# Optimization experiments

Measured on AMD Instinct MI355X. Metric: run time of the kernel, lower is better.

## Reference

```python
import jax, jax.numpy as jnp
import numpy as np

NUM_GROUPS = 32
EPS = 1e-6


def group_norm(x, gamma, beta):
    b, c, h, w = x.shape
    xg = x.reshape(b, NUM_GROUPS, c // NUM_GROUPS, h, w)
    mean = jnp.mean(xg, axis=(2, 3, 4), keepdims=True)
    var = jnp.var(xg, axis=(2, 3, 4), keepdims=True)
    xg = (xg - mean) * jax.lax.rsqrt(var + EPS)
    x = xg.reshape(b, c, h, w)
    return x * gamma[None, :, None, None] + beta[None, :, None, None]


def conv1x1(x, w, b):
    # x: [B,C,H,W], w: [Cout,Cin], b: [Cout]
    return jnp.einsum('bchw,oc->bohw', x, w) + b[None, :, None, None]


def setup_inputs() -> dict:
    key = jax.random.key(0)
    ks = jax.random.split(key, 11)
    B, C, H, W = 2, 512, 64, 64
    s = 1.0 / np.sqrt(C)
    return {
        'x': jax.random.normal(ks[0], (B, C, H, W), jnp.float32),
        'norm_gamma': jnp.ones((C,), jnp.float32),
        'norm_beta': jnp.zeros((C,), jnp.float32),
        'wq': jax.random.normal(ks[1], (C, C), jnp.float32) * s,
        'bq': jnp.zeros((C,), jnp.float32),
        'wk': jax.random.normal(ks[2], (C, C), jnp.float32) * s,
        'bk': jnp.zeros((C,), jnp.float32),
        'wv': jax.random.normal(ks[3], (C, C), jnp.float32) * s,
        'bv': jnp.zeros((C,), jnp.float32),
        'wo': jax.random.normal(ks[4], (C, C), jnp.float32) * s,
        'bo': jnp.zeros((C,), jnp.float32),
    }


def reference(x, norm_gamma, norm_beta, wq, bq, wk, bk, wv, bv, wo, bo):
    b, c, h, w = x.shape
    hn = group_norm(x, norm_gamma, norm_beta)
    q = conv1x1(hn, wq, bq).reshape(b, c, h * w)  # [B,C,HW]
    k = conv1x1(hn, wk, bk).reshape(b, c, h * w)
    v = conv1x1(hn, wv, bv).reshape(b, c, h * w)
    scale = jnp.asarray(c, x.dtype) ** -0.5
    # scores[b,i,j] = sum_c q[b,c,i] * k[b,c,j]
    scores = jnp.einsum('bci,bcj->bij', q, k) * scale
    attn = jax.nn.softmax(scores, axis=2)
    # out[b,c,i] = sum_j v[b,c,j] * attn[b,i,j]
    out = jnp.einsum('bcj,bij->bci', v, attn).reshape(b, c, h, w)
    out = conv1x1(out, wo, bo)
    return x + out
```

## Files before the change

### kernel.cpp

```cpp
#include <hip/hip_runtime.h>
#include <hip/hip_bf16.h>

using u16 = unsigned short;
typedef __attribute__((ext_vector_type(4))) float f32x4;
typedef __attribute__((ext_vector_type(8))) __bf16 bf16x8;
typedef __attribute__((ext_vector_type(8))) short s16x8;
typedef __attribute__((ext_vector_type(4))) short s16x4;

#define DEVI __device__ __forceinline__

constexpr int BATCH = 2, C = 512, HW = 4096, NG = 32, CPG = 16;

DEVI float b2f(u16 u) { union { unsigned u; float f; } a; a.u = ((unsigned)u) << 16; return a.f; }
DEVI u16 f2b(float f) {
  union { float f; unsigned u; } a; a.f = f;
  unsigned r = a.u + 0x7fffu + ((a.u >> 16) & 1u);
  return (u16)(r >> 16);
}

__global__ __launch_bounds__(256) void cvt_w(const float* __restrict__ a, const float* __restrict__ b,
                                             const float* __restrict__ c, const float* __restrict__ d,
                                             u16* __restrict__ out) {
  int i = blockIdx.x * 256 + threadIdx.x;
  int w = i >> 16;
  int off = (i & 65535) * 4;
  const float* s = (w == 0) ? a : (w == 1) ? b : (w == 2) ? c : d;
  f32x4 v = *(const f32x4*)(s + off);
  s16x4 o;
  o[0] = (short)f2b(v[0]); o[1] = (short)f2b(v[1]); o[2] = (short)f2b(v[2]); o[3] = (short)f2b(v[3]);
  *(s16x4*)(out + (size_t)w * 262144 + off) = o;
}

__global__ __launch_bounds__(1024) void gn_stats(const float* __restrict__ x, float* __restrict__ stats) {
  int bg = blockIdx.x;
  const f32x4* xg = (const f32x4*)(x + (size_t)bg * (CPG * HW));
  float s = 0.f, ss = 0.f;
  for (int i = threadIdx.x; i < CPG * HW / 4; i += 1024) {
    f32x4 v = xg[i];
    s += v[0] + v[1] + v[2] + v[3];
    ss += v[0] * v[0] + v[1] * v[1] + v[2] * v[2] + v[3] * v[3];
  }
  #pragma unroll
  for (int o = 32; o; o >>= 1) { s += __shfl_xor(s, o); ss += __shfl_xor(ss, o); }
  __shared__ float red[32];
  int wv = threadIdx.x >> 6, ln = threadIdx.x & 63;
  if (ln == 0) { red[wv] = s; red[16 + wv] = ss; }
  __syncthreads();
  if (threadIdx.x == 0) {
    float S = 0.f, SS = 0.f;
    for (int i = 0; i < 16; ++i) { S += red[i]; SS += red[16 + i]; }
    float inv = 1.f / (float)(CPG * HW);
    float mean = S * inv;
    float var = SS * inv - mean * mean;
    stats[bg * 2] = mean;
    stats[bg * 2 + 1] = rsqrtf(var + 1e-6f);
  }
}

__global__ __launch_bounds__(256) void gn_normT(const float* __restrict__ x, const float* __restrict__ stats,
                                                const float* __restrict__ gamma, const float* __restrict__ beta,
                                                u16* __restrict__ hnT) {
  __shared__ u16 tile[64][66];
  int b = blockIdx.z, c0 = blockIdx.y * 64, h0 = blockIdx.x * 64;
  int t = threadIdx.x;
  const float* xb = x + ((size_t)b * C + c0) * HW + h0;
  int r = t / 16, cc = (t % 16) * 4;
  #pragma unroll
  for (int it = 0; it < 4; ++it) {
    int rr = it * 16 + r;
    int ch = c0 + rr;
    int g = b * NG + (ch >> 4);
    float mean = stats[g * 2], rstd = stats[g * 2 + 1];
    float ga = gamma[ch] * rstd;
    float be = beta[ch] - mean * ga;
    f32x4 v = *(const f32x4*)(xb + (size_t)rr * HW + cc);
    #pragma unroll
    for (int j = 0; j < 4; ++j) tile[rr][cc + j] = f2b(v[j] * ga + be);
  }
  __syncthreads();
  u16* op = hnT + (size_t)b * HW * C + (size_t)h0 * C + c0;
  int hr2 = t / 8, cg = (t % 8) * 8;
  #pragma unroll
  for (int it = 0; it < 2; ++it) {
    int hr = it * 32 + hr2;
    s16x8 o8;
    #pragma unroll
    for (int j = 0; j < 8; ++j) o8[j] = (short)tile[cg + j][hr];
    *(s16x8*)(op + (size_t)hr * C + cg) = o8;
  }
}

#define EPI_BIAS_M 1
#define EPI_BIAS_N 2
#define EPI_RESID  4
#define EPI_F32OUT 8

template <int EPI>
__global__ __launch_bounds__(256) void gemm_bt(const u16* __restrict__ A, const u16* __restrict__ Bt,
                                               void* __restrict__ Co, int M, int N, int K,
                                               long long sA, long long sB, long long sC,
                                               const float* __restrict__ bias,
                                               const float* __restrict__ resid, long long sR) {
  (void)M;
  __shared__ u16 ldsA[128 * 64];
  __shared__ u16 ldsB[128 * 64];
  const int tid = threadIdx.x;
  const int bz = blockIdx.z;
  const int bm = blockIdx.y, bn = blockIdx.x;
  A += (size_t)bz * sA;
  Bt += (size_t)bz * sB;
  const int wave = tid >> 6, lane = tid & 63;
  const int wr = wave >> 1, wc = wave & 1;
  f32x4 acc[4][4] = {};

  const int srow = tid >> 3;
  const int sch = (tid & 7) ^ (srow & 7);
  const u16* gA = A + (size_t)(bm * 128 + srow) * K + sch * 8;
  const u16* gB = Bt + (size_t)(bn * 128 + srow) * K + sch * 8;
  u16* lA = ldsA + wave * 512;
  u16* lB = ldsB + wave * 512;

  for (int k0 = 0; k0 < K; k0 += 64) {
    #pragma unroll
    for (int cc = 0; cc < 4; ++cc) {
      __builtin_amdgcn_global_load_lds(
          (const __attribute__((address_space(1))) void*)(gA + (size_t)cc * 32 * K + k0),
          (__attribute__((address_space(3))) void*)(lA + cc * 2048), 16, 0, 0);
      __builtin_amdgcn_global_load_lds(
          (const __attribute__((address_space(1))) void*)(gB + (size_t)cc * 32 * K + k0),
          (__attribute__((address_space(3))) void*)(lB + cc * 2048), 16, 0, 0);
    }
    __syncthreads();
    #pragma unroll
    for (int kk = 0; kk < 2; ++kk) {
      bf16x8 af[4], bfv[4];
      #pragma unroll
      for (int m = 0; m < 4; ++m) {
        int r = wr * 64 + m * 16 + (lane & 15);
        int chunk = (kk * 4 + (lane >> 4)) ^ (r & 7);
        af[m] = *(const bf16x8*)(ldsA + r * 64 + chunk * 8);
      }
      #pragma unroll
      for (int n = 0; n < 4; ++n) {
        int r = wc * 64 + n * 16 + (lane & 15);
        int chunk = (kk * 4 + (lane >> 4)) ^ (r & 7);
        bfv[n] = *(const bf16x8*)(ldsB + r * 64 + chunk * 8);
      }
      #pragma unroll
      for (int m = 0; m < 4; ++m)
        #pragma unroll
        for (int n = 0; n < 4; ++n)
          acc[m][n] = __builtin_amdgcn_mfma_f32_16x16x32_bf16(af[m], bfv[n], acc[m][n], 0, 0, 0);
    }
    __syncthreads();
  }

  const int col0 = bn * 128 + wc * 64;
  const int row0 = bm * 128 + wr * 64 + ((lane >> 4) << 2);
  #pragma unroll
  for (int m = 0; m < 4; ++m) {
    #pragma unroll
    for (int j = 0; j < 4; ++j) {
      int gm = row0 + m * 16 + j;
      float bm_v = (EPI & EPI_BIAS_M) ? bias[gm] : 0.f;
      #pragma unroll
      for (int n = 0; n < 4; ++n) {
        int gn = col0 + n * 16 + (lane & 15);
        float v = acc[m][n][j] + bm_v;
        if (EPI & EPI_BIAS_N) v += bias[gn];
        if (EPI & EPI_RESID) v += resid[(size_t)bz * sR + (size_t)gm * N + gn];
        if (EPI & EPI_F32OUT)
          ((float*)Co)[(size_t)bz * sC + (size_t)gm * N + gn] = v;
        else
          ((u16*)Co)[(size_t)bz * sC + (size_t)gm * N + gn] = f2b(v);
      }
    }
  }
}

template <bool SCALED>
__global__ __launch_bounds__(512, 2) void gemm256(
    const u16* __restrict__ Ag, const u16* __restrict__ Bg,
    u16* __restrict__ Co, u16* __restrict__ Co2, int zSwitch,
    int Nld, int ldK, int nsplitLog, int kLen,
    long long sA, long long sB, long long sC, float scale) {
  __shared__ u16 lds[65536];
  const int tid = threadIdx.x;
  const int lane = tid & 63, w = tid >> 6;
  const int wm = w >> 2, wn = w & 3;
  const int l15 = lane & 15, l4 = lane >> 4;
  const int bn = blockIdx.x, bm = blockIdx.y;
  const int z = blockIdx.z;
  const int bz = z >> nsplitLog, kz = z & ((1 << nsplitLog) - 1);
  const int kStart = kz * kLen;
  const int NT = kLen >> 6;

  const int rStage = w * 8 + (lane >> 3);
  const int gch = (lane & 7) ^ (lane >> 3);
  const u16* gA = Ag + (size_t)bz * sA + (size_t)(bm * 256) * ldK + kStart + gch * 8;
  const u16* gB = Bg + (size_t)bz * sB + (size_t)(bn * 256) * ldK + kStart + gch * 8;

  f32x4 acc[8][4] = {};
  bf16x8 aF[4][2], bF[2][2][2];

  const int hB = wn >> 1, qB = wn & 1;
  const u16* pA0 = lds + (0 * 4 + wm) * 8192;
  const u16* pA1 = lds + (1 * 4 + wm) * 8192;
  const u16* pB0 = lds + (0 * 4 + 2 + hB) * 8192;
  const u16* pB1 = lds + (1 * 4 + 2 + hB) * 8192;

  #define STAGE(TT, DB, AB, HF) { \
    const u16* gbase = (AB) ? gB : gA; \
    u16* l0 = lds + ((DB) * 4 + (AB) * 2 + (HF)) * 8192 + w * 512; \
    _Pragma("unroll") for (int s = 0; s < 2; ++s) { \
      const u16* gp = gbase + (size_t)((HF) * 128 + s * 64 + rStage) * ldK + (TT) * 64; \
      __builtin_amdgcn_global_load_lds((const __attribute__((address_space(1))) void*)gp, \
          (__attribute__((address_space(3))) void*)(l0 + s * 4096), 16, 0, 0); } }

  #define LOAD_A(P, MH) { _Pragma("unroll") for (int j = 0; j < 4; ++j) \
    _Pragma("unroll") for (int kk = 0; kk < 2; ++kk) { \
      const int r_ = (MH) * 64 + j * 16 + l15; const int c_ = (kk * 4 + l4) ^ (r_ & 7); \
      aF[j][kk] = *(const bf16x8*)((P) + r_ * 64 + c_ * 8); } }

  #define LOAD_B(P, NH) { _Pragma("unroll") for (int j = 0; j < 2; ++j) \
    _Pragma("unroll") for (int kk = 0; kk < 2; ++kk) { \
      const int r_ = qB * 64 + (NH) * 32 + j * 16 + l15; const int c_ = (kk * 4 + l4) ^ (r_ & 7); \
      bF[NH][j][kk] = *(const bf16x8*)((P) + r_ * 64 + c_ * 8); } }

  #define MM(MH, NH) { __builtin_amdgcn_s_setprio(1); \
    _Pragma("unroll") for (int j = 0; j < 4; ++j) \
      _Pragma("unroll") for (int j2 = 0; j2 < 2; ++j2) \
        _Pragma("unroll") for (int kk = 0; kk < 2; ++kk) \
          acc[(MH) * 4 + j][(NH) * 2 + j2] = __builtin_amdgcn_mfma_f32_16x16x32_bf16( \
              aF[j][kk], bF[NH][j2][kk], acc[(MH) * 4 + j][(NH) * 2 + j2], 0, 0, 0); \
    __builtin_amdgcn_s_setprio(0); }

  #define BAR __builtin_amdgcn_s_barrier()
  #define WLG { asm volatile("s_waitcnt lgkmcnt(0)" ::: "memory"); __builtin_amdgcn_sched_barrier(0); }
  #define WV4 asm volatile("s_waitcnt vmcnt(4)" ::: "memory")
  #define WV0 asm volatile("s_waitcnt vmcnt(0)" ::: "memory")

  STAGE(0, 0, 1, 0); STAGE(0, 0, 1, 1);
  STAGE(0, 0, 0, 0); STAGE(0, 0, 0, 1);
  STAGE(1, 1, 1, 0); STAGE(1, 1, 1, 1);
  WV4; BAR;

  const int NI = NT / 2 - 1;
  for (int i = 0; i < NI; ++i) {
    const int t1 = 2 * i + 1, u0 = 2 * i + 2, u1 = 2 * i + 3;
    LOAD_A(pA0, 0); LOAD_B(pB0, 0); STAGE(t1, 1, 0, 0); BAR; WLG; MM(0, 0); BAR;
    LOAD_B(pB0, 1); STAGE(t1, 1, 0, 1); BAR; WLG; MM(0, 1); BAR;
    LOAD_A(pA0, 1); STAGE(u0, 0, 1, 0); BAR; WLG; MM(1, 1); BAR;
    STAGE(u0, 0, 1, 1); BAR; WLG; MM(1, 0); WV4; BAR;
    LOAD_A(pA1, 0); LOAD_B(pB1, 0); STAGE(u0, 0, 0, 0); BAR; WLG; MM(0, 0); BAR;
    LOAD_B(pB1, 1); STAGE(u0, 0, 0, 1); BAR; WLG; MM(0, 1); BAR;
    LOAD_A(pA1, 1); STAGE(u1, 1, 1, 0); BAR; WLG; MM(1, 1); BAR;
    STAGE(u1, 1, 1, 1); BAR; WLG; MM(1, 0); WV4; BAR;
  }
  {
    const int t1 = NT - 1;
    LOAD_A(pA0, 0); LOAD_B(pB0, 0); STAGE(t1, 1, 0, 0); BAR; WLG; MM(0, 0); BAR;
    LOAD_B(pB0, 1); STAGE(t1, 1, 0, 1); BAR; WLG; MM(0, 1); BAR;
    LOAD_A(pA0, 1); BAR; WLG; MM(1, 1); BAR;
    BAR; WLG; MM(1, 0); WV0; BAR;
    LOAD_A(pA1, 0); LOAD_B(pB1, 0); BAR; WLG; MM(0, 0); BAR;
    LOAD_B(pB1, 1); BAR; WLG; MM(0, 1); BAR;
    LOAD_A(pA1, 1); BAR; WLG; MM(1, 1); BAR;
    MM(1, 0);
  }
  #undef STAGE
  #undef LOAD_A
  #undef LOAD_B
  #undef MM
  #undef BAR
  #undef WLG
  #undef WV4
  #undef WV0

  u16* outp = (z < zSwitch) ? (Co + (size_t)z * sC) : (Co2 + (size_t)(z - zSwitch) * sC);
  const int gm0 = bm * 256 + wm * 128 + l4 * 4;
  const int gn0 = bn * 256 + wn * 64 + l15;
  #pragma unroll
  for (int m = 0; m < 8; ++m) {
    #pragma unroll
    for (int j = 0; j < 4; ++j) {
      const size_t rowoff = (size_t)(gm0 + m * 16 + j) * Nld;
      #pragma unroll
      for (int n = 0; n < 4; ++n) {
        float v = acc[m][n][j];
        if (SCALED) v *= scale;
        outp[rowoff + gn0 + n * 16] = f2b(v);
      }
    }
  }
}

__global__ __launch_bounds__(256) void softmax_rows(u16* __restrict__ S) {
  int row = blockIdx.x * 4 + (threadIdx.x >> 6);
  int lane = threadIdx.x & 63;
  s16x8* p = (s16x8*)(S + (size_t)row * 4096);
  float v[64];
  float m = -1e30f;
  #pragma unroll
  for (int j = 0; j < 8; ++j) {
    s16x8 raw = p[j * 64 + lane];
    #pragma unroll
    for (int e = 0; e < 8; ++e) {
      float f = b2f((u16)raw[e]);
      v[j * 8 + e] = f;
      m = fmaxf(m, f);
    }
  }
  #pragma unroll
  for (int o = 32; o; o >>= 1) m = fmaxf(m, __shfl_xor(m, o));
  float s = 0.f;
  #pragma unroll
  for (int i = 0; i < 64; ++i) { v[i] = __expf(v[i] - m); s += v[i]; }
  #pragma unroll
  for (int o = 32; o; o >>= 1) s += __shfl_xor(s, o);
  float r = 1.f / s;
  #pragma unroll
  for (int j = 0; j < 8; ++j) {
    s16x8 o8;
    #pragma unroll
    for (int e = 0; e < 8; ++e) o8[e] = (short)f2b(v[j * 8 + e] * r);
    p[j * 64 + lane] = o8;
  }
}

__global__ __launch_bounds__(256) void reduce_pv(const u16* __restrict__ P, const u16* __restrict__ P2,
                                                 u16* __restrict__ ao) {
  const size_t e = ((size_t)blockIdx.x * 256 + threadIdx.x) * 8;
  const int b = (int)(e >> 21);
  const size_t o = e & 2097151;
  float s[8] = {0.f, 0.f, 0.f, 0.f, 0.f, 0.f, 0.f, 0.f};
  #pragma unroll
  for (int kz = 0; kz < 4; ++kz) {
    const int zz = b * 4 + kz;
    const u16* src = (zz < 6) ? (P + (size_t)zz * 2097152) : (P2 + (size_t)(zz - 6) * 2097152);
    s16x8 v = *(const s16x8*)(src + o);
    #pragma unroll
    for (int j = 0; j < 8; ++j) s[j] += b2f((u16)v[j]);
  }
  s16x8 o8;
  #pragma unroll
  for (int j = 0; j < 8; ++j) o8[j] = (short)f2b(s[j]);
  *(s16x8*)(ao + e) = o8;
}

extern "C" void kernel_launch(void* const* d_in, const int* in_sizes, int n_in,
                              void* d_out, int out_size, void* d_ws, size_t ws_size,
                              hipStream_t stream) {
  (void)in_sizes; (void)n_in; (void)out_size; (void)ws_size;
  const float* x     = (const float*)d_in[0];
  const float* gamma = (const float*)d_in[1];
  const float* beta  = (const float*)d_in[2];
  const float* wq    = (const float*)d_in[3];
  const float* bq    = (const float*)d_in[4];
  const float* wk    = (const float*)d_in[5];
  const float* bk    = (const float*)d_in[6];
  const float* wv    = (const float*)d_in[7];
  const float* bv    = (const float*)d_in[8];
  const float* wo    = (const float*)d_in[9];
  const float* bo    = (const float*)d_in[10];

  char* ws = (char*)d_ws;
  const size_t MiB = 1024 * 1024;
  float* stats = (float*)ws;
  u16* wbf = (u16*)(ws + 1024);
  u16* vv  = (u16*)(ws + 4 * MiB);
  u16* hnT = (u16*)(ws + 12 * MiB);
  u16* qT  = (u16*)(ws + 20 * MiB);
  u16* kT  = (u16*)(ws + 28 * MiB);
  u16* Ppart = (u16*)(ws + 12 * MiB);
  u16* Sm  = (u16*)(ws + 36 * MiB);
  u16* aoT = (u16*)(ws + 36 * MiB);

  const long long sTok = (long long)HW * C;
  const long long sS   = (long long)HW * HW;
  const float scale = 0.044194173824159216f;

  cvt_w<<<dim3(1024), dim3(256), 0, stream>>>(wq, wk, wv, wo, wbf);
  gn_stats<<<dim3(64), dim3(1024), 0, stream>>>(x, stats);
  gn_normT<<<dim3(HW / 64, C / 64, BATCH), dim3(256), 0, stream>>>(x, stats, gamma, beta, hnT);

  gemm_bt<EPI_BIAS_N><<<dim3(4, 32, BATCH), dim3(256), 0, stream>>>(
      hnT, wbf + 0 * 262144, qT, HW, C, C, sTok, 0, sTok, bq, nullptr, 0);
  gemm_bt<EPI_BIAS_N><<<dim3(4, 32, BATCH), dim3(256), 0, stream>>>(
      hnT, wbf + 1 * 262144, kT, HW, C, C, sTok, 0, sTok, bk, nullptr, 0);
  gemm_bt<EPI_BIAS_M><<<dim3(32, 4, BATCH), dim3(256), 0, stream>>>(
      wbf + 2 * 262144, hnT, vv, C, HW, C, 0, sTok, sTok, bv, nullptr, 0);

  gemm256<true><<<dim3(16, 16, BATCH), dim3(512), 0, stream>>>(
      qT, kT, Sm, Sm, 1000, HW, C, 0, C, sTok, sTok, sS, scale);

  softmax_rows<<<dim3(2048), dim3(256), 0, stream>>>(Sm);

  gemm256<false><<<dim3(2, 16, BATCH * 4), dim3(512), 0, stream>>>(
      Sm, vv, Ppart, (u16*)d_out, 6, C, HW, 2, HW / 4, sS, sTok, (long long)2097152, 1.f);

  reduce_pv<<<dim3(2048), dim3(256), 0, stream>>>(Ppart, (const u16*)d_out, aoT);

  gemm_bt<EPI_BIAS_M | EPI_RESID | EPI_F32OUT><<<dim3(32, 4, BATCH), dim3(256), 0, stream>>>(
      wbf + 3 * 262144, aoT, d_out, C, HW, C, 0, sTok, (long long)C * HW, bo, x, (long long)C * HW);
}
```

Before: 190.7 us.

## Fuse Q/K projections, remap workgroups across XCDs, stage gemm256 epilogue through LDS

Q and K projections now run as one GEMM against the concatenated wq|wk weights, writing an interleaved [HW,1024] buffer. This removes a launch and a second read of hnT. All GEMMs remap flat block IDs so that consecutive tiles land on the same XCD, which should improve L2 reuse. The 256x256 GEMM epilogue now writes to swizzled LDS and then stores coalesced 16-byte vectors instead of scattered 2-byte stores. The costs are wider strides for the QK^T reads and an extra LDS round trip with a barrier.

Result: faster. 178.9 us (-6.2%).

```diff
diff --git a/kernel.cpp b/kernel.cpp
--- a/kernel.cpp
+++ b/kernel.cpp
@@ -16,6 +16,18 @@
   union { float f; unsigned u; } a; a.f = f;
   unsigned r = a.u + 0x7fffu + ((a.u >> 16) & 1u);
   return (u16)(r >> 16);
+}
+
+DEVI void xcd_remap(int& bx, int& by, int& bz) {
+  const int nx = gridDim.x, ny = gridDim.y;
+  const int nwg = nx * ny * gridDim.z;
+  const int flat = blockIdx.x + nx * (blockIdx.y + ny * blockIdx.z);
+  const int cpx = nwg >> 3;
+  const int w = (flat & 7) * cpx + (flat >> 3);
+  bx = w % nx;
+  const int t = w / nx;
+  by = t % ny;
+  bz = t / ny;
 }
 
 __global__ __launch_bounds__(256) void cvt_w(const float* __restrict__ a, const float* __restrict__ b,
@@ -94,19 +106,21 @@
 #define EPI_BIAS_N 2
 #define EPI_RESID  4
 #define EPI_F32OUT 8
+#define EPI_QK     32
 
 template <int EPI>
 __global__ __launch_bounds__(256) void gemm_bt(const u16* __restrict__ A, const u16* __restrict__ Bt,
                                                void* __restrict__ Co, int M, int N, int K,
                                                long long sA, long long sB, long long sC,
                                                const float* __restrict__ bias,
+                                               const float* __restrict__ biasB,
                                                const float* __restrict__ resid, long long sR) {
   (void)M;
   __shared__ u16 ldsA[128 * 64];
   __shared__ u16 ldsB[128 * 64];
   const int tid = threadIdx.x;
-  const int bz = blockIdx.z;
-  const int bm = blockIdx.y, bn = blockIdx.x;
+  int bn, bm, bz;
+  xcd_remap(bn, bm, bz);
   A += (size_t)bz * sA;
   Bt += (size_t)bz * sB;
   const int wave = tid >> 6, lane = tid & 63;
@@ -167,7 +181,10 @@
       for (int n = 0; n < 4; ++n) {
         int gn = col0 + n * 16 + (lane & 15);
         float v = acc[m][n][j] + bm_v;
-        if (EPI & EPI_BIAS_N) v += bias[gn];
+        if (EPI & EPI_BIAS_N) {
+          if (EPI & EPI_QK) v += (gn < 512) ? bias[gn] : biasB[gn - 512];
+          else v += bias[gn];
+        }
         if (EPI & EPI_RESID) v += resid[(size_t)bz * sR + (size_t)gm * N + gn];
         if (EPI & EPI_F32OUT)
           ((float*)Co)[(size_t)bz * sC + (size_t)gm * N + gn] = v;
@@ -189,8 +206,8 @@
   const int lane = tid & 63, w = tid >> 6;
   const int wm = w >> 2, wn = w & 3;
   const int l15 = lane & 15, l4 = lane >> 4;
-  const int bn = blockIdx.x, bm = blockIdx.y;
-  const int z = blockIdx.z;
+  int bn, bm, z;
+  xcd_remap(bn, bm, z);
   const int bz = z >> nsplitLog, kz = z & ((1 << nsplitLog) - 1);
   const int kStart = kz * kLen;
   const int NT = kLen >> 6;
@@ -277,20 +294,32 @@
   #undef WV4
   #undef WV0
 
-  u16* outp = (z < zSwitch) ? (Co + (size_t)z * sC) : (Co2 + (size_t)(z - zSwitch) * sC);
-  const int gm0 = bm * 256 + wm * 128 + l4 * 4;
-  const int gn0 = bn * 256 + wn * 64 + l15;
-  #pragma unroll
-  for (int m = 0; m < 8; ++m) {
-    #pragma unroll
-    for (int j = 0; j < 4; ++j) {
-      const size_t rowoff = (size_t)(gm0 + m * 16 + j) * Nld;
+  {
+    const int rloc = wm * 128 + l4 * 4;
+    const int cloc = wn * 64 + l15;
+    #pragma unroll
+    for (int m = 0; m < 8; ++m) {
       #pragma unroll
-      for (int n = 0; n < 4; ++n) {
-        float v = acc[m][n][j];
-        if (SCALED) v *= scale;
-        outp[rowoff + gn0 + n * 16] = f2b(v);
+      for (int j = 0; j < 4; ++j) {
+        const int r_ = rloc + m * 16 + j;
+        const int xr = ((r_ >> 2) & 3) << 5;
+        #pragma unroll
+        for (int n = 0; n < 4; ++n) {
+          float v = acc[m][n][j];
+          if (SCALED) v *= scale;
+          *(u16*)((char*)lds + ((r_ * 512 + (cloc + n * 16) * 2) ^ xr)) = f2b(v);
+        }
       }
+    }
+    __syncthreads();
+    u16* outp = (z < zSwitch) ? (Co + (size_t)z * sC) : (Co2 + (size_t)(z - zSwitch) * sC);
+    #pragma unroll
+    for (int it = 0; it < 16; ++it) {
+      const int idx = it * 512 + tid;
+      const int r_ = idx >> 5, ch = idx & 31;
+      const int xr = ((r_ >> 2) & 3) << 5;
+      s16x8 d8 = *(const s16x8*)((const char*)lds + ((r_ * 512 + ch * 16) ^ xr));
+      *(s16x8*)(outp + (size_t)(bm * 256 + r_) * Nld + bn * 256 + ch * 8) = d8;
     }
   }
 }
@@ -369,30 +398,28 @@
   float* stats = (float*)ws;
   u16* wbf = (u16*)(ws + 1024);
   u16* vv  = (u16*)(ws + 4 * MiB);
-  u16* hnT = (u16*)(ws + 12 * MiB);
-  u16* qT  = (u16*)(ws + 20 * MiB);
-  u16* kT  = (u16*)(ws + 28 * MiB);
+  u16* qkT = (u16*)(ws + 12 * MiB);
+  u16* hnT = (u16*)(ws + 28 * MiB);
   u16* Ppart = (u16*)(ws + 12 * MiB);
   u16* Sm  = (u16*)(ws + 36 * MiB);
   u16* aoT = (u16*)(ws + 36 * MiB);
 
-  const long long sTok = (long long)HW * C;
-  const long long sS   = (long long)HW * HW;
+  const long long sTok  = (long long)HW * C;
+  const long long sTok2 = (long long)HW * 1024;
+  const long long sS    = (long long)HW * HW;
   const float scale = 0.044194173824159216f;
 
   cvt_w<<<dim3(1024), dim3(256), 0, stream>>>(wq, wk, wv, wo, wbf);
   gn_stats<<<dim3(64), dim3(1024), 0, stream>>>(x, stats);
   gn_normT<<<dim3(HW / 64, C / 64, BATCH), dim3(256), 0, stream>>>(x, stats, gamma, beta, hnT);
 
-  gemm_bt<EPI_BIAS_N><<<dim3(4, 32, BATCH), dim3(256), 0, stream>>>(
-      hnT, wbf + 0 * 262144, qT, HW, C, C, sTok, 0, sTok, bq, nullptr, 0);
-  gemm_bt<EPI_BIAS_N><<<dim3(4, 32, BATCH), dim3(256), 0, stream>>>(
-      hnT, wbf + 1 * 262144, kT, HW, C, C, sTok, 0, sTok, bk, nullptr, 0);
+  gemm_bt<EPI_BIAS_N | EPI_QK><<<dim3(8, 32, BATCH), dim3(256), 0, stream>>>(
+      hnT, wbf, qkT, HW, 1024, C, sTok, 0, sTok2, bq, bk, nullptr, 0);
   gemm_bt<EPI_BIAS_M><<<dim3(32, 4, BATCH), dim3(256), 0, stream>>>(
-      wbf + 2 * 262144, hnT, vv, C, HW, C, 0, sTok, sTok, bv, nullptr, 0);
+      wbf + 2 * 262144, hnT, vv, C, HW, C, 0, sTok, sTok, bv, nullptr, nullptr, 0);
 
   gemm256<true><<<dim3(16, 16, BATCH), dim3(512), 0, stream>>>(
-      qT, kT, Sm, Sm, 1000, HW, C, 0, C, sTok, sTok, sS, scale);
+      qkT, qkT + 512, Sm, Sm, 1000, HW, 1024, 0, C, sTok2, sTok2, sS, scale);
 
   softmax_rows<<<dim3(2048), dim3(256), 0, stream>>>(Sm);
 
@@ -402,5 +429,5 @@
   reduce_pv<<<dim3(2048), dim3(256), 0, stream>>>(Ppart, (const u16*)d_out, aoT);
 
   gemm_bt<EPI_BIAS_M | EPI_RESID | EPI_F32OUT><<<dim3(32, 4, BATCH), dim3(256), 0, stream>>>(
-      wbf + 3 * 262144, aoT, d_out, C, HW, C, 0, sTok, (long long)C * HW, bo, x, (long long)C * HW);
-}
+      wbf + 3 * 262144, aoT, d_out, C, HW, C, 0, sTok, (long long)C * HW, bo, nullptr, x, (long long)C * HW);
+}
```
